# Performance work log

Measured on AMD Instinct MI355X. Metric: run time of the kernel, lower is better.

The kernel has to match this reference:

```python
import jax, jax.numpy as jnp
import numpy as np

B, R, NM, H, P1, G1, RC1, LAT = 16384, 360, 200, 256, 512, 256, 256, 128


def _linear_params(k, out_f, in_f):
    s = 1.0 / np.sqrt(in_f)
    kw, kb = jax.random.split(k)
    W = jax.random.uniform(kw, (out_f, in_f), minval=-s, maxval=s, dtype=jnp.float32)
    b = jax.random.uniform(kb, (out_f,), minval=-s, maxval=s, dtype=jnp.float32)
    return W, b


def setup_inputs() -> dict:
    key = jax.random.key(0)
    ks = jax.random.split(key, 14)
    x_window = jax.random.normal(ks[0], (B, 3, R), dtype=jnp.float32)
    modes = jax.random.normal(ks[1], (R, NM), dtype=jnp.float32)
    mode_coeff = jax.random.normal(ks[2], (B, NM), dtype=jnp.float32)
    W1, b1 = _linear_params(ks[3], H, 3 * R)      # surrogate layer 1
    W2, b2 = _linear_params(ks[4], H, H)          # surrogate layer 2
    W3, b3 = _linear_params(ks[5], R, H)          # surrogate layer 3
    Wp1, bp1 = _linear_params(ks[6], P1, R * R)   # npi_proj
    Wp2, bp2 = _linear_params(ks[7], LAT, P1)
    Wg1, bg1 = _linear_params(ks[8], G1, NM)      # geo_proj
    Wg2, bg2 = _linear_params(ks[9], LAT, G1)
    Wr1, br1 = _linear_params(ks[10], RC1, LAT)   # recon
    Wr2, br2 = _linear_params(ks[11], R, RC1)
    return dict(x_window=x_window, modes=modes, mode_coeff=mode_coeff,
                W1=W1, b1=b1, W2=W2, b2=b2, W3=W3, b3=b3,
                Wp1=Wp1, bp1=bp1, Wp2=Wp2, bp2=bp2,
                Wg1=Wg1, bg1=bg1, Wg2=Wg2, bg2=bg2,
                Wr1=Wr1, br1=br1, Wr2=Wr2, br2=br2)


def reference(x_window, modes, mode_coeff,
              W1, b1, W2, b2, W3, b3,
              Wp1, bp1, Wp2, bp2,
              Wg1, bg1, Wg2, bg2,
              Wr1, br1, Wr2, br2):
    Bs = x_window.shape[0]
    Rr = W3.shape[0]
    # ---- NPI surrogate forward (needed for ReLU masks) ----
    z = x_window.reshape(Bs, 3 * Rr)                       # (B, 3R)
    h1 = z @ W1.T + b1                                     # (B, H)
    m1 = (h1 > 0).astype(z.dtype)
    h2 = (h1 * m1) @ W2.T + b2                             # (B, H)
    m2 = (h2 > 0).astype(z.dtype)
    # ---- EC: exact batch-mean Jacobian of the ReLU MLP w.r.t last timestep ----
    # mean_b [ W3 diag(m2_b) W2 diag(m1_b) W1_last ] = W3 @ (W2 * (m2^T m1 / B)) @ W1[:, -R:]
    G = (m2.T @ m1) / Bs                                   # (H, H)
    ec = W3 @ ((W2 * G) @ W1[:, -Rr:])                     # (R, R); row j = dy_j/dx
    ec = jax.lax.stop_gradient(ec)                         # create_graph=False in original
    # ---- projections ----
    ec_flat = ec.reshape(1, Rr * Rr)
    z_npi1 = jax.nn.relu(ec_flat @ Wp1.T + bp1) @ Wp2.T + bp2   # (1, LAT)
    z_npi = jnp.tile(z_npi1, (Bs, 1))                           # (B, LAT)
    z_geo = jax.nn.relu(mode_coeff @ Wg1.T + bg1) @ Wg2.T + bg2  # (B, LAT)
    zsum = z_npi + z_geo
    zn = zsum / jnp.maximum(jnp.linalg.norm(zsum, axis=-1, keepdims=True), 1e-12)
    recon = jax.nn.relu(zn @ Wr1.T + br1) @ Wr2.T + br2          # (B, R)
    return (z_npi, z_geo, zn, ec, recon)
```

## Files before the change

kernel.cpp:

```cpp
#include <hip/hip_runtime.h>

typedef __bf16 bf16x8 __attribute__((ext_vector_type(8)));
typedef __bf16 bf16x4 __attribute__((ext_vector_type(4)));
typedef float  f32x4  __attribute__((ext_vector_type(4)));

__device__ __forceinline__ f32x4 mfma_bf16(bf16x8 a, bf16x8 b, f32x4 c) {
  return __builtin_amdgcn_mfma_f32_16x16x32_bf16(a, b, c, 0, 0, 0);
}
__device__ __forceinline__ bf16x8 ldB(const __bf16* Bp, int kt, int NT, int nt,
                                      int lane) {
  return *reinterpret_cast<const bf16x8*>(Bp + (((size_t)kt * NT + nt) * 64 + lane) * 8);
}

__device__ __forceinline__ void gridbar(int* cnt, int target) {
  __syncthreads();
  if (threadIdx.x == 0) {
    __threadfence();
    __hip_atomic_fetch_add(cnt, 1, __ATOMIC_RELEASE, __HIP_MEMORY_SCOPE_AGENT);
    while (__hip_atomic_load(cnt, __ATOMIC_RELAXED, __HIP_MEMORY_SCOPE_AGENT) < target)
      __builtin_amdgcn_s_sleep(4);
    __threadfence();
  }
  __syncthreads();
}

__global__ void pack_all(const float* __restrict__ W1, const float* __restrict__ W2,
                         const float* __restrict__ Wg1, const float* __restrict__ Wg2,
                         const float* __restrict__ Wr1, const float* __restrict__ Wr2,
                         __bf16* __restrict__ W1p, __bf16* __restrict__ W2p,
                         __bf16* __restrict__ Wg1p, __bf16* __restrict__ Wg2p,
                         __bf16* __restrict__ Wr1p, __bf16* __restrict__ Wr2p,
                         float* __restrict__ G, int* __restrict__ cnt) {
  int bx = blockIdx.x;
  int lane = threadIdx.x;
  if (bx >= 1104) {
    if (bx == 1104 && lane == 0) cnt[0] = 0;
    float4* g = (float4*)G;
    int base = (bx - 1104) * 512 + lane;
#pragma unroll
    for (int i = 0; i < 8; ++i) g[base + i * 64] = make_float4(0.f, 0.f, 0.f, 0.f);
    return;
  }
  const float* W; __bf16* out; int N, K, NT, local;
  if (bx < 544)      { W = W1;  out = W1p;  N = 256; K = 1080; NT = 16; local = bx; }
  else if (bx < 672) { W = W2;  out = W2p;  N = 256; K = 256;  NT = 16; local = bx - 544; }
  else if (bx < 784) { W = Wg1; out = Wg1p; N = 256; K = 200;  NT = 16; local = bx - 672; }
  else if (bx < 848) { W = Wg2; out = Wg2p; N = 128; K = 256;  NT = 8;  local = bx - 784; }
  else if (bx < 912) { W = Wr1; out = Wr1p; N = 256; K = 128;  NT = 16; local = bx - 848; }
  else               { W = Wr2; out = Wr2p; N = 360; K = 256;  NT = 24; local = bx - 912; }
  int nt = local % NT, kt = local / NT;
  int n = nt * 16 + (lane & 15);
  int k0 = kt * 32 + (lane >> 4) * 8;
  bf16x8 v;
#pragma unroll
  for (int e = 0; e < 8; ++e) {
    int k = k0 + e;
    float xv = (n < N && k < K) ? W[(size_t)n * K + k] : 0.f;
    v[e] = (__bf16)xv;
  }
  *reinterpret_cast<bf16x8*>(out + ((size_t)local * 64 + lane) * 8) = v;
}

__global__ __launch_bounds__(256) void h1h2_fused(
    const float* __restrict__ x, const __bf16* __restrict__ W1p,
    const float* __restrict__ b1, const __bf16* __restrict__ W2p,
    const float* __restrict__ b2, __bf16* __restrict__ m1T,
    __bf16* __restrict__ m2T) {
  __shared__ __bf16 Alds[32][68];
  __shared__ __bf16 h1s[32][264];
  int tid = threadIdx.x;
  int lane = tid & 63, wid = tid >> 6;
  int rowBase = blockIdx.x * 32;
  int sr = tid >> 3, sc = (tid & 7) * 8;
  const float* aSrc = x + (size_t)(rowBase + sr) * 1080;
  f32x4 acc[2][4] = {};
  float4 c0a, c0b, c1a, c1b;
  auto LD = [&](int s, float4& a, float4& b) {
    int gk = s * 64 + sc;
    if (gk < 1080) {
      a = *(const float4*)(aSrc + gk);
      b = *(const float4*)(aSrc + gk + 4);
    } else {
      a = make_float4(0.f, 0.f, 0.f, 0.f);
      b = a;
    }
  };
  LD(0, c0a, c0b);
  LD(1, c1a, c1b);
  for (int s = 0; s < 17; ++s) {
    bf16x8 w8;
    w8[0] = (__bf16)c0a.x; w8[1] = (__bf16)c0a.y; w8[2] = (__bf16)c0a.z; w8[3] = (__bf16)c0a.w;
    w8[4] = (__bf16)c0b.x; w8[5] = (__bf16)c0b.y; w8[6] = (__bf16)c0b.z; w8[7] = (__bf16)c0b.w;
    *reinterpret_cast<bf16x8*>(&Alds[sr][sc]) = w8;
    __syncthreads();
    c0a = c1a; c0b = c1b;
    if (s + 2 < 17) LD(s + 2, c1a, c1b);
    int arow = lane & 15;
#pragma unroll
    for (int ks = 0; ks < 2; ++ks) {
      int ak = ks * 32 + (lane >> 4) * 8;
      bf16x8 a0 = *reinterpret_cast<const bf16x8*>(&Alds[arow][ak]);
      bf16x8 a1 = *reinterpret_cast<const bf16x8*>(&Alds[arow + 16][ak]);
      int kt = s * 2 + ks;
#pragma unroll
      for (int n = 0; n < 4; ++n) {
        bf16x8 bv = ldB(W1p, kt, 16, wid * 4 + n, lane);
        acc[0][n] = mfma_bf16(a0, bv, acc[0][n]);
        acc[1][n] = mfma_bf16(a1, bv, acc[1][n]);
      }
    }
    __syncthreads();
  }
  int q4 = (lane >> 4) * 4;
#pragma unroll
  for (int m = 0; m < 2; ++m)
#pragma unroll
    for (int n = 0; n < 4; ++n) {
      int col = wid * 64 + n * 16 + (lane & 15);
      float bb = b1[col];
#pragma unroll
      for (int j = 0; j < 4; ++j) {
        int rl = m * 16 + q4 + j;
        float h = acc[m][n][j] + bb;
        m1T[(size_t)col * 16384 + rowBase + rl] = (__bf16)(h > 0.f ? 1.f : 0.f);
        h1s[rl][col] = (__bf16)fmaxf(h, 0.f);
      }
    }
  __syncthreads();
  f32x4 acc2[2][4] = {};
#pragma unroll
  for (int ks = 0; ks < 8; ++ks) {
    int arow = lane & 15, ak = ks * 32 + (lane >> 4) * 8;
    bf16x8 a0 = *reinterpret_cast<const bf16x8*>(&h1s[arow][ak]);
    bf16x8 a1 = *reinterpret_cast<const bf16x8*>(&h1s[arow + 16][ak]);
#pragma unroll
    for (int n = 0; n < 4; ++n) {
      bf16x8 bv = ldB(W2p, ks, 16, wid * 4 + n, lane);
      acc2[0][n] = mfma_bf16(a0, bv, acc2[0][n]);
      acc2[1][n] = mfma_bf16(a1, bv, acc2[1][n]);
    }
  }
#pragma unroll
  for (int m = 0; m < 2; ++m)
#pragma unroll
    for (int n = 0; n < 4; ++n) {
      int col = wid * 64 + n * 16 + (lane & 15);
      float bb = b2[col];
#pragma unroll
      for (int j = 0; j < 4; ++j) {
        int rl = m * 16 + q4 + j;
        float h = acc2[m][n][j] + bb;
        m2T[(size_t)col * 16384 + rowBase + rl] = (__bf16)(h > 0.f ? 1.f : 0.f);
      }
    }
}

__global__ __launch_bounds__(256) void gemm_masks(
    const __bf16* __restrict__ m2T, const __bf16* __restrict__ m1T,
    float* __restrict__ G) {
  int tid = threadIdx.x;
  int lane = tid & 63, wid = tid >> 6;
  int wr = wid >> 1, wc = wid & 1;
  int ibase = blockIdx.x * 64, jbase = blockIdx.y * 64;
  size_t b0 = (size_t)blockIdx.z * 1024 + (lane >> 4) * 8;
  const __bf16* pa0 = m2T + (size_t)(ibase + wr * 32 + (lane & 15)) * 16384 + b0;
  const __bf16* pa1 = pa0 + (size_t)16 * 16384;
  const __bf16* pb0 = m1T + (size_t)(jbase + wc * 32 + (lane & 15)) * 16384 + b0;
  const __bf16* pb1 = pb0 + (size_t)16 * 16384;
  f32x4 acc[2][2] = {};
#pragma unroll 4
  for (int c = 0; c < 32; ++c) {
    bf16x8 a0 = *reinterpret_cast<const bf16x8*>(pa0 + c * 32);
    bf16x8 a1 = *reinterpret_cast<const bf16x8*>(pa1 + c * 32);
    bf16x8 bv0 = *reinterpret_cast<const bf16x8*>(pb0 + c * 32);
    bf16x8 bv1 = *reinterpret_cast<const bf16x8*>(pb1 + c * 32);
    acc[0][0] = mfma_bf16(a0, bv0, acc[0][0]);
    acc[0][1] = mfma_bf16(a0, bv1, acc[0][1]);
    acc[1][0] = mfma_bf16(a1, bv0, acc[1][0]);
    acc[1][1] = mfma_bf16(a1, bv1, acc[1][1]);
  }
  int q4 = (lane >> 4) * 4;
#pragma unroll
  for (int m = 0; m < 2; ++m)
#pragma unroll
    for (int n = 0; n < 2; ++n)
#pragma unroll
      for (int j = 0; j < 4; ++j) {
        int gi = ibase + wr * 32 + m * 16 + q4 + j;
        int gj = jbase + wc * 32 + n * 16 + (lane & 15);
        atomicAdd(&G[(size_t)gi * 256 + gj], acc[m][n][j] * (1.f / 16384.f));
      }
}

__device__ void small_body(float (*As)[17], float (*Bs)[65], int t,
                           const float* __restrict__ A, const float* __restrict__ A2,
                           int lda, const float* __restrict__ Bm, int ldb,
                           float* __restrict__ C, int ldc,
                           int M, int N, int K, int m0, int n0) {
  int tx = t & 15, ty = t >> 4;
  float acc[4][4] = {};
  for (int k0 = 0; k0 < K; k0 += 16) {
#pragma unroll
    for (int i = 0; i < 4; ++i) {
      int idx = t * 4 + i;
      int r = idx >> 4, kk = idx & 15;
      int gm = m0 + r, gk = k0 + kk;
      float v = (gm < M && gk < K) ? A[(size_t)gm * lda + gk] : 0.f;
      if (A2 && gm < M && gk < K) v *= A2[(size_t)gm * lda + gk];
      As[r][kk] = v;
      int kk2 = idx >> 6, cc = idx & 63;
      int gk2 = k0 + kk2, gn = n0 + cc;
      Bs[kk2][cc] = (gk2 < K && gn < N) ? Bm[(size_t)gk2 * ldb + gn] : 0.f;
    }
    __syncthreads();
#pragma unroll
    for (int kk = 0; kk < 16; ++kk)
#pragma unroll
      for (int i = 0; i < 4; ++i)
#pragma unroll
        for (int j = 0; j < 4; ++j)
          acc[i][j] += As[ty * 4 + i][kk] * Bs[kk][tx * 4 + j];
    __syncthreads();
  }
#pragma unroll
  for (int i = 0; i < 4; ++i)
#pragma unroll
    for (int j = 0; j < 4; ++j) {
      int gm = m0 + ty * 4 + i, gn = n0 + tx * 4 + j;
      if (gm < M && gn < N) C[(size_t)gm * ldc + gn] = acc[i][j];
    }
}

__global__ __launch_bounds__(256) void small_pair(
    const float* __restrict__ W2, const float* __restrict__ G,
    const float* __restrict__ W1, const float* __restrict__ W3,
    float* __restrict__ T, float* __restrict__ o_ec, int* __restrict__ cnt) {
  __shared__ float As[64][17];
  __shared__ float Bs[16][65];
  int t = threadIdx.x, bid = blockIdx.x;
  if (bid < 24)
    small_body(As, Bs, t, W2, G, 256, W1 + 720, 1080, T, 384,
               256, 360, 256, (bid / 6) * 64, (bid % 6) * 64);
  gridbar(cnt, 36);
  small_body(As, Bs, t, W3, nullptr, 256, T, 384, o_ec, 360,
             360, 360, 256, (bid / 6) * 64, (bid % 6) * 64);
}

__global__ __launch_bounds__(512) void p_and_g1(
    const float* __restrict__ Wp1, const float* __restrict__ ec,
    const float* __restrict__ bp1, float* __restrict__ p,
    const float* __restrict__ mc, const __bf16* __restrict__ Wg1p,
    const float* __restrict__ bg1, const __bf16* __restrict__ Wg2p,
    const float* __restrict__ bg2, float* __restrict__ o_zgeo) {
  __shared__ __bf16 Alds[64][40];
  __shared__ __bf16 g1S[64][264];
  __shared__ float redw[8];
  int t = threadIdx.x;
  if (blockIdx.x < 512) {
    int row = blockIdx.x;
    const float4* w = (const float4*)(Wp1 + (size_t)row * 129600);
    const float4* e = (const float4*)ec;
    float s = 0.f;
    for (int i = t; i < 32400; i += 512) {
      float4 a = w[i], b = e[i];
      s += a.x * b.x + a.y * b.y + a.z * b.z + a.w * b.w;
    }
    for (int o = 32; o; o >>= 1) s += __shfl_down(s, o);
    if ((t & 63) == 0) redw[t >> 6] = s;
    __syncthreads();
    if (t == 0) {
      float tot = 0.f;
#pragma unroll
      for (int i = 0; i < 8; ++i) tot += redw[i];
      p[row] = fmaxf(tot + bp1[row], 0.f);
    }
  } else {
    int lane = t & 63, wid = t >> 6;
    int wr = wid >> 2, wc = wid & 3;
    int rowBase = (blockIdx.x - 512) * 64;
    int sr = t >> 3, sc = (t & 7) * 4;
    const float* aSrc = mc + (size_t)(rowBase + sr) * 200;
    int q4 = (lane >> 4) * 4;
    f32x4 acc[2][4] = {};
    for (int kt = 0; kt < 7; ++kt) {
      int gk = kt * 32 + sc;
      bf16x4 w4;
      if (gk < 200) {
        float4 v = *(const float4*)(aSrc + gk);
        w4[0] = (__bf16)v.x; w4[1] = (__bf16)v.y;
        w4[2] = (__bf16)v.z; w4[3] = (__bf16)v.w;
      } else {
        w4[0] = w4[1] = w4[2] = w4[3] = (__bf16)0.f;
      }
      *reinterpret_cast<bf16x4*>(&Alds[sr][sc]) = w4;
      __syncthreads();
      int arow = wr * 32 + (lane & 15), ak = (lane >> 4) * 8;
      bf16x8 a0 = *reinterpret_cast<const bf16x8*>(&Alds[arow][ak]);
      bf16x8 a1 = *reinterpret_cast<const bf16x8*>(&Alds[arow + 16][ak]);
#pragma unroll
      for (int n = 0; n < 4; ++n) {
        bf16x8 bv = ldB(Wg1p, kt, 16, wc * 4 + n, lane);
        acc[0][n] = mfma_bf16(a0, bv, acc[0][n]);
        acc[1][n] = mfma_bf16(a1, bv, acc[1][n]);
      }
      __syncthreads();
    }
#pragma unroll
    for (int m = 0; m < 2; ++m)
#pragma unroll
      for (int n = 0; n < 4; ++n) {
        int col = wc * 64 + n * 16 + (lane & 15);
        float bb = bg1[col];
#pragma unroll
        for (int j = 0; j < 4; ++j) {
          int rl = wr * 32 + m * 16 + q4 + j;
          g1S[rl][col] = (__bf16)fmaxf(acc[m][n][j] + bb, 0.f);
        }
      }
    __syncthreads();
    f32x4 acc2[2][2] = {};
#pragma unroll
    for (int ks = 0; ks < 8; ++ks) {
      int arow = wr * 32 + (lane & 15), ak = ks * 32 + (lane >> 4) * 8;
      bf16x8 a0 = *reinterpret_cast<const bf16x8*>(&g1S[arow][ak]);
      bf16x8 a1 = *reinterpret_cast<const bf16x8*>(&g1S[arow + 16][ak]);
#pragma unroll
      for (int n = 0; n < 2; ++n) {
        bf16x8 bv = ldB(Wg2p, ks, 8, wc * 2 + n, lane);
        acc2[0][n] = mfma_bf16(a0, bv, acc2[0][n]);
        acc2[1][n] = mfma_bf16(a1, bv, acc2[1][n]);
      }
    }
#pragma unroll
    for (int m = 0; m < 2; ++m)
#pragma unroll
      for (int n = 0; n < 2; ++n) {
        int col = wc * 32 + n * 16 + (lane & 15);
        float bb = bg2[col];
#pragma unroll
        for (int j = 0; j < 4; ++j) {
          int row = rowBase + wr * 32 + m * 16 + q4 + j;
          o_zgeo[(size_t)row * 128 + col] = acc2[m][n][j] + bb;
        }
      }
  }
}

__global__ __launch_bounds__(512) void mega_tail(
    const float* __restrict__ p, const float* __restrict__ Wp2,
    const float* __restrict__ bp2, const float* __restrict__ zgeo,
    const __bf16* __restrict__ Wr1p, const float* __restrict__ br1,
    const __bf16* __restrict__ Wr2p, const float* __restrict__ br2,
    float* __restrict__ o_znpi, float* __restrict__ o_zn,
    float* __restrict__ o_rec) {
  __shared__ __bf16 r1S[64][264];
  __shared__ __bf16 znS[64][136];
  __shared__ float znpiS[128];
  __shared__ float pS[512];
  int tid = threadIdx.x;
  int lane = tid & 63, wid = tid >> 6;
  int wr = wid >> 2, wc = wid & 3;
  int rowBase = blockIdx.x * 64;
  int q4 = (lane >> 4) * 4;
  pS[tid] = p[tid];
  __syncthreads();
  {
    int col = tid >> 2, q = tid & 3;
    const float4* w = (const float4*)(Wp2 + (size_t)col * 512 + q * 128);
    const float4* pv = (const float4*)(pS + q * 128);
    float s = 0.f;
#pragma unroll
    for (int i = 0; i < 32; ++i) {
      float4 a = w[i], b = pv[i];
      s += a.x * b.x + a.y * b.y + a.z * b.z + a.w * b.w;
    }
    s += __shfl_xor(s, 1);
    s += __shfl_xor(s, 2);
    if (q == 0) znpiS[col] = s + bp2[col];
  }
  __syncthreads();
  {
    int rg = tid >> 5;
    int c4 = (tid & 31) * 4;
    float4 zp = make_float4(znpiS[c4], znpiS[c4 + 1], znpiS[c4 + 2], znpiS[c4 + 3]);
#pragma unroll
    for (int ri = 0; ri < 4; ++ri) {
      int rl = rg + ri * 16;
      int row = rowBase + rl;
      float4 zg = *(const float4*)(zgeo + (size_t)row * 128 + c4);
      float4 zs = make_float4(zg.x + zp.x, zg.y + zp.y, zg.z + zp.z, zg.w + zp.w);
      *(float4*)(o_znpi + (size_t)row * 128 + c4) = zp;
      float ss = zs.x * zs.x + zs.y * zs.y + zs.z * zs.z + zs.w * zs.w;
      ss += __shfl_xor(ss, 1);
      ss += __shfl_xor(ss, 2);
      ss += __shfl_xor(ss, 4);
      ss += __shfl_xor(ss, 8);
      ss += __shfl_xor(ss, 16);
      float rn = 1.f / fmaxf(sqrtf(ss), 1e-12f);
      float4 zn = make_float4(zs.x * rn, zs.y * rn, zs.z * rn, zs.w * rn);
      *(float4*)(o_zn + (size_t)row * 128 + c4) = zn;
      bf16x4 znb;
      znb[0] = (__bf16)zn.x; znb[1] = (__bf16)zn.y;
      znb[2] = (__bf16)zn.z; znb[3] = (__bf16)zn.w;
      *reinterpret_cast<bf16x4*>(&znS[rl][c4]) = znb;
    }
  }
  __syncthreads();
  {
    f32x4 acc[2][4] = {};
#pragma unroll
    for (int ks = 0; ks < 4; ++ks) {
      int arow = wr * 32 + (lane & 15), ak = ks * 32 + (lane >> 4) * 8;
      bf16x8 a0 = *reinterpret_cast<const bf16x8*>(&znS[arow][ak]);
      bf16x8 a1 = *reinterpret_cast<const bf16x8*>(&znS[arow + 16][ak]);
#pragma unroll
      for (int n = 0; n < 4; ++n) {
        bf16x8 bv = ldB(Wr1p, ks, 16, wc * 4 + n, lane);
        acc[0][n] = mfma_bf16(a0, bv, acc[0][n]);
        acc[1][n] = mfma_bf16(a1, bv, acc[1][n]);
      }
    }
#pragma unroll
    for (int m = 0; m < 2; ++m)
#pragma unroll
      for (int n = 0; n < 4; ++n) {
        int col = wc * 64 + n * 16 + (lane & 15);
        float bb = br1[col];
#pragma unroll
        for (int j = 0; j < 4; ++j) {
          int rl = wr * 32 + m * 16 + q4 + j;
          r1S[rl][col] = (__bf16)fmaxf(acc[m][n][j] + bb, 0.f);
        }
      }
  }
  __syncthreads();
  {
    f32x4 acc[2][6] = {};
#pragma unroll
    for (int ks = 0; ks < 8; ++ks) {
      int arow = wr * 32 + (lane & 15), ak = ks * 32 + (lane >> 4) * 8;
      bf16x8 a0 = *reinterpret_cast<const bf16x8*>(&r1S[arow][ak]);
      bf16x8 a1 = *reinterpret_cast<const bf16x8*>(&r1S[arow + 16][ak]);
#pragma unroll
      for (int n = 0; n < 6; ++n) {
        bf16x8 bv = ldB(Wr2p, ks, 24, wc * 6 + n, lane);
        acc[0][n] = mfma_bf16(a0, bv, acc[0][n]);
        acc[1][n] = mfma_bf16(a1, bv, acc[1][n]);
      }
    }
#pragma unroll
    for (int m = 0; m < 2; ++m)
#pragma unroll
      for (int n = 0; n < 6; ++n) {
        int col = wc * 96 + n * 16 + (lane & 15);
        if (col < 360) {
          float bb = br2[col];
#pragma unroll
          for (int j = 0; j < 4; ++j) {
            int rl = wr * 32 + m * 16 + q4 + j;
            o_rec[(size_t)(rowBase + rl) * 360 + col] = acc[m][n][j] + bb;
          }
        }
      }
  }
}

extern "C" void kernel_launch(void* const* d_in, const int* in_sizes, int n_in,
                              void* d_out, int out_size, void* d_ws,
                              size_t ws_size, hipStream_t stream) {
  (void)in_sizes; (void)n_in; (void)out_size; (void)ws_size;
  const float* x   = (const float*)d_in[0];
  const float* mc  = (const float*)d_in[2];
  const float* W1  = (const float*)d_in[3];  const float* b1  = (const float*)d_in[4];
  const float* W2  = (const float*)d_in[5];  const float* b2  = (const float*)d_in[6];
  const float* W3  = (const float*)d_in[7];
  const float* Wp1 = (const float*)d_in[9];  const float* bp1 = (const float*)d_in[10];
  const float* Wp2 = (const float*)d_in[11]; const float* bp2 = (const float*)d_in[12];
  const float* Wg1 = (const float*)d_in[13]; const float* bg1 = (const float*)d_in[14];
  const float* Wg2 = (const float*)d_in[15]; const float* bg2 = (const float*)d_in[16];
  const float* Wr1 = (const float*)d_in[17]; const float* br1 = (const float*)d_in[18];
  const float* Wr2 = (const float*)d_in[19]; const float* br2 = (const float*)d_in[20];

  float* out = (float*)d_out;
  float* o_znpi = out;
  float* o_zgeo = out + 2097152;
  float* o_zn   = out + 4194304;
  float* o_ec   = out + 6291456;
  float* o_rec  = out + 6421056;

  char* ws = (char*)d_ws;
  __bf16* m1T   = (__bf16*)(ws + 0);
  __bf16* m2T   = (__bf16*)(ws + 8388608);
  float*  G     = (float*)(ws + 16777216);
  float*  T     = (float*)(ws + 17039360);
  float*  p512  = (float*)(ws + 17432576);
  __bf16* W1p   = (__bf16*)(ws + 17434624);
  __bf16* W2p   = W1p  + (size_t)544 * 512;
  __bf16* Wg1p  = W2p  + (size_t)128 * 512;
  __bf16* Wg2p  = Wg1p + (size_t)112 * 512;
  __bf16* Wr1p  = Wg2p + (size_t)64 * 512;
  __bf16* Wr2p  = Wr1p + (size_t)64 * 512;
  int*    cnt   = (int*)(ws + 18565120);

  pack_all<<<1136, 64, 0, stream>>>(W1, W2, Wg1, Wg2, Wr1, Wr2,
                                    W1p, W2p, Wg1p, Wg2p, Wr1p, Wr2p, G, cnt);
  h1h2_fused<<<512, 256, 0, stream>>>(x, W1p, b1, W2p, b2, m1T, m2T);
  gemm_masks<<<dim3(4, 4, 16), 256, 0, stream>>>(m2T, m1T, G);
  small_pair<<<36, 256, 0, stream>>>(W2, G, W1, W3, T, o_ec, cnt);
  p_and_g1<<<768, 512, 0, stream>>>(Wp1, o_ec, bp1, p512, mc, Wg1p, bg1,
                                    Wg2p, bg2, o_zgeo);
  mega_tail<<<256, 512, 0, stream>>>(p512, Wp2, bp2, o_zgeo, Wr1p, br1,
                                     Wr2p, br2, o_znpi, o_zn, o_rec);
}
```

Baseline: 261.2 us.

## Load GEMM A operands directly to registers and stage mask stores through LDS

In the h1/h2 kernel and the geo-projection branch, each wave now loads its A-fragment rows straight from global memory into registers and converts them to bf16, dropping the shared-memory staging tile and its per-step barriers. The h1h2 kernel also writes its ReLU masks into a transposed LDS tile first, then stores them to m1T/m2T as contiguous 16-byte rows. Before, each element went out as a scattered 2-byte write with a 32 KB stride. The goal is fewer LDS barriers and coalesced mask writes. The cost is that all four waves now load the same A rows redundantly, and cross-thread reuse of A is lost.

```diff
diff --git a/kernel.cpp b/kernel.cpp
--- a/kernel.cpp
+++ b/kernel.cpp
@@ -10,6 +10,12 @@
 __device__ __forceinline__ bf16x8 ldB(const __bf16* Bp, int kt, int NT, int nt,
                                       int lane) {
   return *reinterpret_cast<const bf16x8*>(Bp + (((size_t)kt * NT + nt) * 64 + lane) * 8);
+}
+__device__ __forceinline__ bf16x8 cvt8(float4 a, float4 b) {
+  bf16x8 v;
+  v[0] = (__bf16)a.x; v[1] = (__bf16)a.y; v[2] = (__bf16)a.z; v[3] = (__bf16)a.w;
+  v[4] = (__bf16)b.x; v[5] = (__bf16)b.y; v[6] = (__bf16)b.z; v[7] = (__bf16)b.w;
+  return v;
 }
 
 __device__ __forceinline__ void gridbar(int* cnt, int target) {
@@ -66,52 +72,38 @@
     const float* __restrict__ b1, const __bf16* __restrict__ W2p,
     const float* __restrict__ b2, __bf16* __restrict__ m1T,
     __bf16* __restrict__ m2T) {
-  __shared__ __bf16 Alds[32][68];
   __shared__ __bf16 h1s[32][264];
+  __shared__ __bf16 mskT[256][40];
   int tid = threadIdx.x;
   int lane = tid & 63, wid = tid >> 6;
   int rowBase = blockIdx.x * 32;
-  int sr = tid >> 3, sc = (tid & 7) * 8;
-  const float* aSrc = x + (size_t)(rowBase + sr) * 1080;
+  int q4 = (lane >> 4) * 4;
+  int kg = (lane >> 4) * 8;
+  const float* a0p = x + (size_t)(rowBase + (lane & 15)) * 1080;
+  const float* a1p = a0p + (size_t)16 * 1080;
   f32x4 acc[2][4] = {};
-  float4 c0a, c0b, c1a, c1b;
-  auto LD = [&](int s, float4& a, float4& b) {
-    int gk = s * 64 + sc;
-    if (gk < 1080) {
-      a = *(const float4*)(aSrc + gk);
-      b = *(const float4*)(aSrc + gk + 4);
+#pragma unroll 2
+  for (int kt = 0; kt < 34; ++kt) {
+    int k0 = kt * 32 + kg;
+    bf16x8 a0, a1;
+    if (k0 < 1080) {
+      float4 x0 = *(const float4*)(a0p + k0);
+      float4 x1 = *(const float4*)(a0p + k0 + 4);
+      float4 y0 = *(const float4*)(a1p + k0);
+      float4 y1 = *(const float4*)(a1p + k0 + 4);
+      a0 = cvt8(x0, x1);
+      a1 = cvt8(y0, y1);
     } else {
-      a = make_float4(0.f, 0.f, 0.f, 0.f);
-      b = a;
-    }
-  };
-  LD(0, c0a, c0b);
-  LD(1, c1a, c1b);
-  for (int s = 0; s < 17; ++s) {
-    bf16x8 w8;
-    w8[0] = (__bf16)c0a.x; w8[1] = (__bf16)c0a.y; w8[2] = (__bf16)c0a.z; w8[3] = (__bf16)c0a.w;
-    w8[4] = (__bf16)c0b.x; w8[5] = (__bf16)c0b.y; w8[6] = (__bf16)c0b.z; w8[7] = (__bf16)c0b.w;
-    *reinterpret_cast<bf16x8*>(&Alds[sr][sc]) = w8;
-    __syncthreads();
-    c0a = c1a; c0b = c1b;
-    if (s + 2 < 17) LD(s + 2, c1a, c1b);
-    int arow = lane & 15;
-#pragma unroll
-    for (int ks = 0; ks < 2; ++ks) {
-      int ak = ks * 32 + (lane >> 4) * 8;
-      bf16x8 a0 = *reinterpret_cast<const bf16x8*>(&Alds[arow][ak]);
-      bf16x8 a1 = *reinterpret_cast<const bf16x8*>(&Alds[arow + 16][ak]);
-      int kt = s * 2 + ks;
-#pragma unroll
-      for (int n = 0; n < 4; ++n) {
-        bf16x8 bv = ldB(W1p, kt, 16, wid * 4 + n, lane);
-        acc[0][n] = mfma_bf16(a0, bv, acc[0][n]);
-        acc[1][n] = mfma_bf16(a1, bv, acc[1][n]);
-      }
-    }
-    __syncthreads();
-  }
-  int q4 = (lane >> 4) * 4;
+#pragma unroll
+      for (int e = 0; e < 8; ++e) { a0[e] = (__bf16)0.f; a1[e] = (__bf16)0.f; }
+    }
+#pragma unroll
+    for (int n = 0; n < 4; ++n) {
+      bf16x8 bv = ldB(W1p, kt, 16, wid * 4 + n, lane);
+      acc[0][n] = mfma_bf16(a0, bv, acc[0][n]);
+      acc[1][n] = mfma_bf16(a1, bv, acc[1][n]);
+    }
+  }
 #pragma unroll
   for (int m = 0; m < 2; ++m)
 #pragma unroll
@@ -122,11 +114,18 @@
       for (int j = 0; j < 4; ++j) {
         int rl = m * 16 + q4 + j;
         float h = acc[m][n][j] + bb;
-        m1T[(size_t)col * 16384 + rowBase + rl] = (__bf16)(h > 0.f ? 1.f : 0.f);
+        mskT[col][rl] = (__bf16)(h > 0.f ? 1.f : 0.f);
         h1s[rl][col] = (__bf16)fmaxf(h, 0.f);
       }
     }
   __syncthreads();
+  {
+    __bf16* dst = m1T + (size_t)tid * 16384 + rowBase;
+#pragma unroll
+    for (int i = 0; i < 4; ++i)
+      *reinterpret_cast<bf16x8*>(dst + i * 8) =
+          *reinterpret_cast<const bf16x8*>(&mskT[tid][i * 8]);
+  }
   f32x4 acc2[2][4] = {};
 #pragma unroll
   for (int ks = 0; ks < 8; ++ks) {
@@ -140,6 +139,7 @@
       acc2[1][n] = mfma_bf16(a1, bv, acc2[1][n]);
     }
   }
+  __syncthreads();
 #pragma unroll
   for (int m = 0; m < 2; ++m)
 #pragma unroll
@@ -150,9 +150,17 @@
       for (int j = 0; j < 4; ++j) {
         int rl = m * 16 + q4 + j;
         float h = acc2[m][n][j] + bb;
-        m2T[(size_t)col * 16384 + rowBase + rl] = (__bf16)(h > 0.f ? 1.f : 0.f);
-      }
-    }
+        mskT[col][rl] = (__bf16)(h > 0.f ? 1.f : 0.f);
+      }
+    }
+  __syncthreads();
+  {
+    __bf16* dst = m2T + (size_t)tid * 16384 + rowBase;
+#pragma unroll
+    for (int i = 0; i < 4; ++i)
+      *reinterpret_cast<bf16x8*>(dst + i * 8) =
+          *reinterpret_cast<const bf16x8*>(&mskT[tid][i * 8]);
+  }
 }
 
 __global__ __launch_bounds__(256) void gemm_masks(
@@ -252,7 +260,6 @@
     const float* __restrict__ mc, const __bf16* __restrict__ Wg1p,
     const float* __restrict__ bg1, const __bf16* __restrict__ Wg2p,
     const float* __restrict__ bg2, float* __restrict__ o_zgeo) {
-  __shared__ __bf16 Alds[64][40];
   __shared__ __bf16 g1S[64][264];
   __shared__ float redw[8];
   int t = threadIdx.x;
@@ -278,32 +285,32 @@
     int lane = t & 63, wid = t >> 6;
     int wr = wid >> 2, wc = wid & 3;
     int rowBase = (blockIdx.x - 512) * 64;
-    int sr = t >> 3, sc = (t & 7) * 4;
-    const float* aSrc = mc + (size_t)(rowBase + sr) * 200;
     int q4 = (lane >> 4) * 4;
+    int kg = (lane >> 4) * 8;
+    const float* a0p = mc + (size_t)(rowBase + wr * 32 + (lane & 15)) * 200;
+    const float* a1p = a0p + (size_t)16 * 200;
     f32x4 acc[2][4] = {};
+#pragma unroll
     for (int kt = 0; kt < 7; ++kt) {
-      int gk = kt * 32 + sc;
-      bf16x4 w4;
-      if (gk < 200) {
-        float4 v = *(const float4*)(aSrc + gk);
-        w4[0] = (__bf16)v.x; w4[1] = (__bf16)v.y;
-        w4[2] = (__bf16)v.z; w4[3] = (__bf16)v.w;
+      int k0 = kt * 32 + kg;
+      bf16x8 a0, a1;
+      if (k0 < 200) {
+        float4 x0 = *(const float4*)(a0p + k0);
+        float4 x1 = *(const float4*)(a0p + k0 + 4);
+        float4 y0 = *(const float4*)(a1p + k0);
+        float4 y1 = *(const float4*)(a1p + k0 + 4);
+        a0 = cvt8(x0, x1);
+        a1 = cvt8(y0, y1);
       } else {
-        w4[0] = w4[1] = w4[2] = w4[3] = (__bf16)0.f;
-      }
-      *reinterpret_cast<bf16x4*>(&Alds[sr][sc]) = w4;
-      __syncthreads();
-      int arow = wr * 32 + (lane & 15), ak = (lane >> 4) * 8;
-      bf16x8 a0 = *reinterpret_cast<const bf16x8*>(&Alds[arow][ak]);
-      bf16x8 a1 = *reinterpret_cast<const bf16x8*>(&Alds[arow + 16][ak]);
+#pragma unroll
+        for (int e = 0; e < 8; ++e) { a0[e] = (__bf16)0.f; a1[e] = (__bf16)0.f; }
+      }
 #pragma unroll
       for (int n = 0; n < 4; ++n) {
         bf16x8 bv = ldB(Wg1p, kt, 16, wc * 4 + n, lane);
         acc[0][n] = mfma_bf16(a0, bv, acc[0][n]);
         acc[1][n] = mfma_bf16(a1, bv, acc[1][n]);
       }
-      __syncthreads();
     }
 #pragma unroll
     for (int m = 0; m < 2; ++m)
```

Result: slower. 267.6 us (+2.4%).
